# Kernel optimization log

Measured on AMD Instinct MI355X. Metric: run time of the kernel, lower is better.

## Reference

```python
import jax, jax.numpy as jnp
import numpy as np

N, E, D_LM, H, L, C = 100000, 1000000, 1024, 128, 3, 8


def setup_inputs() -> dict:
    key = jax.random.key(0)
    ks = jax.random.split(key, 8)
    return {
        "last_hidden_state": jax.random.normal(ks[0], (N, D_LM), jnp.float32),
        "edge_index": jax.random.randint(ks[1], (2, E), 0, N, dtype=jnp.int32),
        "W_lm": jax.random.normal(ks[2], (D_LM, H), jnp.float32) * 0.03,
        "b_lm": jnp.zeros((H,), jnp.float32),
        "W_gcn": jax.random.normal(ks[3], (L, H, H), jnp.float32) * 0.08,
        "b_gcn": jnp.zeros((L, H), jnp.float32),
        "W_cls": jax.random.normal(ks[4], (2 * H, C), jnp.float32) * 0.06,
        "b_cls": jnp.zeros((C,), jnp.float32),
    }


def reference(last_hidden_state, edge_index, W_lm, b_lm, W_gcn, b_gcn, W_cls, b_cls):
    # Frozen LM output -> lm_head (dropout is identity in eval mode)
    n = last_hidden_state.shape[0]
    lm = last_hidden_state @ W_lm + b_lm                      # [N, H]

    # GCN normalization (add self-loops, symmetric deg^{-1/2} norm), shared by all layers
    loops = jnp.arange(n, dtype=edge_index.dtype)
    src = jnp.concatenate([edge_index[0], loops])             # message sources j
    dst = jnp.concatenate([edge_index[1], loops])             # aggregation targets i
    deg = jax.ops.segment_sum(jnp.ones_like(dst, jnp.float32), dst, num_segments=n)
    dinv = jax.lax.rsqrt(jnp.maximum(deg, 1.0))               # deg >= 1 due to self-loops
    norm = dinv[src] * dinv[dst]                              # [E+N]

    out = lm
    for l in range(W_gcn.shape[0]):
        h = out @ W_gcn[l]                                    # linear transform first (PyG GCNConv)
        msg = h[src] * norm[:, None]                          # gather + scale  [E+N, H]
        out = jax.ops.segment_sum(msg, dst, num_segments=n) + b_gcn[l]
        out = jax.nn.relu(out)                                # dropout identity in eval

    logits = jnp.concatenate([lm, out], axis=-1) @ W_cls + b_cls  # [N, C]
    return logits
```

## Files before the change

### kernel.cpp

```cpp
#include <hip/hip_runtime.h>


using bf16x8 = __attribute__((ext_vector_type(8))) short;
using f32x4  = __attribute__((ext_vector_type(4))) float;
typedef unsigned short u16;
typedef unsigned int   u32;

__device__ __forceinline__ u16 f2bf(float f) {
  u32 u = __builtin_bit_cast(u32, f);
  u += 0x7fffu + ((u >> 16) & 1u);
  return (u16)(u >> 16);
}
__device__ __forceinline__ float bf2f(u32 lo16) {
  return __builtin_bit_cast(float, lo16 << 16);
}
__device__ __forceinline__ u32 packbf2(float a, float b) {
  return (u32)f2bf(a) | ((u32)f2bf(b) << 16);
}


__global__ void count_kernel(const int* __restrict__ dst, int* __restrict__ counts, int E) {
  int e = blockIdx.x * 256 + threadIdx.x;
  if (e < E) atomicAdd(&counts[dst[e]], 1);
}

__global__ void dinv_kernel(const int* __restrict__ counts, float* __restrict__ dinv, int N) {
  int i = blockIdx.x * 256 + threadIdx.x;
  if (i < N) dinv[i] = rsqrtf((float)(counts[i] + 1));
}

__global__ void scan_partial(const int* __restrict__ counts, int* __restrict__ partials, int N) {
  __shared__ int sdata[256];
  int t = threadIdx.x;
  int base = blockIdx.x * 1024 + t * 4;
  int s = 0;
#pragma unroll
  for (int i = 0; i < 4; i++) { int idx = base + i; if (idx < N) s += counts[idx]; }
  sdata[t] = s; __syncthreads();
  for (int off = 128; off > 0; off >>= 1) {
    if (t < off) sdata[t] += sdata[t + off];
    __syncthreads();
  }
  if (t == 0) partials[blockIdx.x] = sdata[0];
}

__global__ void scan_partials_excl(int* __restrict__ partials, int NB,
                                   int* __restrict__ offsets, int N, int E) {
  __shared__ int sdata[256];
  int t = threadIdx.x;
  int v = (t < NB) ? partials[t] : 0;
  sdata[t] = v; __syncthreads();
  int val = v;
  for (int off = 1; off < 256; off <<= 1) {
    int add = (t >= off) ? sdata[t - off] : 0;
    __syncthreads();
    val += add; sdata[t] = val;
    __syncthreads();
  }
  if (t < NB) partials[t] = val - v;
  if (t == 0) offsets[N] = E;
}

__global__ void scan_final(const int* __restrict__ counts, const int* __restrict__ partials,
                           int* __restrict__ offsets, int N) {
  __shared__ int sdata[256];
  int t = threadIdx.x;
  int base = blockIdx.x * 1024 + t * 4;
  int v[4]; int tsum = 0;
#pragma unroll
  for (int i = 0; i < 4; i++) { int idx = base + i; v[i] = (idx < N) ? counts[idx] : 0; tsum += v[i]; }
  sdata[t] = tsum; __syncthreads();
  int val = tsum;
  for (int off = 1; off < 256; off <<= 1) {
    int add = (t >= off) ? sdata[t - off] : 0;
    __syncthreads();
    val += add; sdata[t] = val;
    __syncthreads();
  }
  int run = partials[blockIdx.x] + val - tsum;
#pragma unroll
  for (int i = 0; i < 4; i++) { int idx = base + i; if (idx < N) offsets[idx] = run; run += v[i]; }
}

__global__ void fill_kernel(const int* __restrict__ src, const int* __restrict__ dst,
                            const int* __restrict__ offsets, int* __restrict__ cursor,
                            const float* __restrict__ dinv,
                            int* __restrict__ col, float* __restrict__ wn, int E) {
  int e = blockIdx.x * 256 + threadIdx.x;
  if (e < E) {
    int d = dst[e], s = src[e];
    int p = offsets[d] + atomicAdd(&cursor[d], 1);
    col[p] = s;
    wn[p] = dinv[s] * dinv[d];
  }
}


__global__ void prep_wlm(const float* __restrict__ W, u16* __restrict__ Wt) {
  int idx = blockIdx.x * 256 + threadIdx.x;
  if (idx < 1024 * 128) {
    int k = idx >> 7, c = idx & 127;
    Wt[c * 1024 + k] = f2bf(W[idx]);
  }
}
__global__ void prep_wgcn(const float* __restrict__ W, u16* __restrict__ Wt, int total) {
  int idx = blockIdx.x * 256 + threadIdx.x;
  if (idx < total) {
    int l = idx >> 14; int r = idx & 16383;
    int k = r >> 7, c = r & 127;
    Wt[l * 16384 + c * 128 + k] = f2bf(W[idx]);
  }
}


template<int K, bool A_IS_F32, bool ADD_BIAS>
__global__ __launch_bounds__(256) void gemm_kernel(
    const void* __restrict__ Aptr, const u16* __restrict__ Bt,
    const float* __restrict__ bias, u16* __restrict__ Out, int Nrows)
{
  __shared__ u16 lA[128 * 32];
  __shared__ u16 lB[128 * 32];
  const int t = threadIdx.x;
  const int lane = t & 63;
  const int w = t >> 6;
  const int wr = w >> 1, wc = w & 1;
  const int row0 = blockIdx.x * 128;
  const int quad = lane >> 4;
  const int l16 = lane & 15;

  f32x4 acc[4][4];
#pragma unroll
  for (int i = 0; i < 4; i++)
#pragma unroll
    for (int j = 0; j < 4; j++) acc[i][j] = f32x4{0.f, 0.f, 0.f, 0.f};

  for (int k0 = 0; k0 < K; k0 += 32) {
    if (A_IS_F32) {
      const float* A = (const float*)Aptr;
#pragma unroll
      for (int rpt = 0; rpt < 2; rpt++) {
        int seg = t + rpt * 256;
        int row = seg >> 2, ks = seg & 3;
        int grow = row0 + row; if (grow >= Nrows) grow = Nrows - 1;
        const float* gp = A + (size_t)grow * K + k0 + ks * 8;
        float4 f0 = *reinterpret_cast<const float4*>(gp);
        float4 f1 = *reinterpret_cast<const float4*>(gp + 4);
        uint4 pk;
        pk.x = packbf2(f0.x, f0.y); pk.y = packbf2(f0.z, f0.w);
        pk.z = packbf2(f1.x, f1.y); pk.w = packbf2(f1.z, f1.w);
        *reinterpret_cast<uint4*>(&lA[seg * 8]) = pk;
      }
    } else {
      const u16* A = (const u16*)Aptr;
#pragma unroll
      for (int rpt = 0; rpt < 2; rpt++) {
        int seg = t + rpt * 256;
        int row = seg >> 2, ks = seg & 3;
        int grow = row0 + row; if (grow >= Nrows) grow = Nrows - 1;
        const u16* gp = A + (size_t)grow * K + k0 + ks * 8;
        *reinterpret_cast<uint4*>(&lA[seg * 8]) = *reinterpret_cast<const uint4*>(gp);
      }
    }
#pragma unroll
    for (int rpt = 0; rpt < 2; rpt++) {
      int seg = t + rpt * 256;
      int c = seg >> 2, ks = seg & 3;
      const u16* gp = Bt + (size_t)c * K + k0 + ks * 8;
      *reinterpret_cast<uint4*>(&lB[seg * 8]) = *reinterpret_cast<const uint4*>(gp);
    }
    __syncthreads();

    bf16x8 af[4], bfr[4];
#pragma unroll
    for (int i = 0; i < 4; i++) {
      int r = wr * 64 + i * 16 + l16;
      af[i] = *reinterpret_cast<const bf16x8*>(&lA[r * 32 + quad * 8]);
    }
#pragma unroll
    for (int j = 0; j < 4; j++) {
      int c = wc * 64 + j * 16 + l16;
      bfr[j] = *reinterpret_cast<const bf16x8*>(&lB[c * 32 + quad * 8]);
    }
    __syncthreads();

#pragma unroll
    for (int i = 0; i < 4; i++)
#pragma unroll
      for (int j = 0; j < 4; j++)
        acc[i][j] = __builtin_amdgcn_mfma_f32_16x16x32_bf16(af[i], bfr[j], acc[i][j], 0, 0, 0);
  }

#pragma unroll
  for (int i = 0; i < 4; i++) {
    int rbase = row0 + wr * 64 + i * 16 + quad * 4;
#pragma unroll
    for (int j = 0; j < 4; j++) {
      int c = wc * 64 + j * 16 + l16;
      float bv = ADD_BIAS ? bias[c] : 0.f;
#pragma unroll
      for (int r = 0; r < 4; r++) {
        int grow = rbase + r;
        if (grow < Nrows) {
          float v = acc[i][j][r] + bv;
          Out[(size_t)grow * 128 + c] = f2bf(v);
        }
      }
    }
  }
}


__global__ __launch_bounds__(256) void aggregate_kernel(
    const u16* __restrict__ h, const int* __restrict__ offsets,
    const int* __restrict__ col, const float* __restrict__ wn,
    const float* __restrict__ dinv, const float* __restrict__ bias,
    u16* __restrict__ outf, int N)
{
  int w = threadIdx.x >> 6;
  int lane = threadIdx.x & 63;
  int i = blockIdx.x * 4 + w;
  if (i >= N) return;
  const u32* h32 = (const u32*)h;
  float di = dinv[i];
  float sw = di * di;
  u32 us = h32[(size_t)i * 64 + lane];
  float ax = sw * bf2f(us & 0xffffu);
  float ay = sw * bf2f(us >> 16);
  int s = offsets[i], e = offsets[i + 1];
  int p = s;
  for (; p + 4 <= e; p += 4) {
    int j0 = col[p], j1 = col[p + 1], j2 = col[p + 2], j3 = col[p + 3];
    float w0 = wn[p], w1 = wn[p + 1], w2 = wn[p + 2], w3 = wn[p + 3];
    u32 u0 = h32[(size_t)j0 * 64 + lane];
    u32 u1 = h32[(size_t)j1 * 64 + lane];
    u32 u2 = h32[(size_t)j2 * 64 + lane];
    u32 u3 = h32[(size_t)j3 * 64 + lane];
    ax += w0 * bf2f(u0 & 0xffffu); ay += w0 * bf2f(u0 >> 16);
    ax += w1 * bf2f(u1 & 0xffffu); ay += w1 * bf2f(u1 >> 16);
    ax += w2 * bf2f(u2 & 0xffffu); ay += w2 * bf2f(u2 >> 16);
    ax += w3 * bf2f(u3 & 0xffffu); ay += w3 * bf2f(u3 >> 16);
  }
  for (; p < e; p++) {
    int j = col[p]; float wv = wn[p];
    u32 uu = h32[(size_t)j * 64 + lane];
    ax += wv * bf2f(uu & 0xffffu); ay += wv * bf2f(uu >> 16);
  }
  ax = fmaxf(ax + bias[lane * 2], 0.f);
  ay = fmaxf(ay + bias[lane * 2 + 1], 0.f);
  ((u32*)outf)[(size_t)i * 64 + lane] = packbf2(ax, ay);
}


__global__ __launch_bounds__(256) void classifier_kernel(
    const u16* __restrict__ lm, const u16* __restrict__ feat,
    const float* __restrict__ Wc, const float* __restrict__ bc,
    float* __restrict__ out, int N)
{
  __shared__ float sW[256 * 8];
  __shared__ u16 sF[32 * 264];
  int t = threadIdx.x;
#pragma unroll
  for (int r = 0; r < 8; r++) sW[t + r * 256] = Wc[t + r * 256];
  int n0 = blockIdx.x * 32;
  u32* sF32 = (u32*)sF;
#pragma unroll
  for (int r = 0; r < 8; r++) {
    int idx = t + r * 256;
    int n = idx >> 6, cpos = idx & 63;
    int gn = n0 + n; if (gn >= N) gn = N - 1;
    sF32[n * 132 + cpos]      = ((const u32*)lm)[(size_t)gn * 64 + cpos];
    sF32[n * 132 + 64 + cpos] = ((const u32*)feat)[(size_t)gn * 64 + cpos];
  }
  __syncthreads();
  int n = t >> 3, c = t & 7;
  int gn = n0 + n;
  float sum = bc[c];
#pragma unroll 16
  for (int k = 0; k < 256; k++)
    sum += bf2f((u32)sF[n * 264 + k]) * sW[k * 8 + c];
  if (gn < N) out[(size_t)gn * 8 + c] = sum;
}


static inline char* bump(char*& p, size_t bytes) {
  char* r = p;
  p += (bytes + 255) & ~(size_t)255;
  return r;
}

extern "C" void kernel_launch(void* const* d_in, const int* in_sizes, int n_in,
                              void* d_out, int out_size, void* d_ws, size_t ws_size,
                              hipStream_t stream) {
  const float* X   = (const float*)d_in[0];
  const int*   EI  = (const int*)  d_in[1];
  const float* Wlm = (const float*)d_in[2];
  const float* blm = (const float*)d_in[3];
  const float* Wg  = (const float*)d_in[4];
  const float* bg  = (const float*)d_in[5];
  const float* Wc  = (const float*)d_in[6];
  const float* bc  = (const float*)d_in[7];
  float* out = (float*)d_out;

  const int N = in_sizes[0] / 1024;
  const int E = in_sizes[1] / 2;
  const int L = in_sizes[4] / (128 * 128);

  char* wp = (char*)d_ws;
  int*   counts  = (int*)  bump(wp, (size_t)N * 4);
  int*   cursor  = (int*)  bump(wp, (size_t)N * 4);
  int*   offs    = (int*)  bump(wp, (size_t)(N + 1) * 4);
  float* dinv    = (float*)bump(wp, (size_t)N * 4);
  int*   partials= (int*)  bump(wp, 1024 * 4);
  int*   colA    = (int*)  bump(wp, (size_t)E * 4);
  float* wnA     = (float*)bump(wp, (size_t)E * 4);
  u16*   WlmT    = (u16*)  bump(wp, (size_t)1024 * 128 * 2);
  u16*   WgT     = (u16*)  bump(wp, (size_t)L * 128 * 128 * 2);
  u16*   lmB     = (u16*)  bump(wp, (size_t)N * 128 * 2);
  u16*   hB      = (u16*)  bump(wp, (size_t)N * 128 * 2);
  u16*   featB   = (u16*)  bump(wp, (size_t)N * 128 * 2);

  hipMemsetAsync(counts, 0, (size_t)N * 4, stream);
  hipMemsetAsync(cursor, 0, (size_t)N * 4, stream);

  const int* srcp = EI;
  const int* dstp = EI + E;

  count_kernel<<<(E + 255) / 256, 256, 0, stream>>>(dstp, counts, E);
  dinv_kernel<<<(N + 255) / 256, 256, 0, stream>>>(counts, dinv, N);

  int NB = (N + 1023) / 1024;
  scan_partial<<<NB, 256, 0, stream>>>(counts, partials, N);
  scan_partials_excl<<<1, 256, 0, stream>>>(partials, NB, offs, N, E);
  scan_final<<<NB, 256, 0, stream>>>(counts, partials, offs, N);
  fill_kernel<<<(E + 255) / 256, 256, 0, stream>>>(srcp, dstp, offs, cursor, dinv, colA, wnA, E);

  prep_wlm<<<(1024 * 128 + 255) / 256, 256, 0, stream>>>(Wlm, WlmT);
  prep_wgcn<<<(L * 128 * 128 + 255) / 256, 256, 0, stream>>>(Wg, WgT, L * 128 * 128);

  int GB = (N + 127) / 128;
  gemm_kernel<1024, true, true><<<GB, 256, 0, stream>>>(X, WlmT, blm, lmB, N);

  const u16* cur = lmB;
  for (int l = 0; l < L; l++) {
    gemm_kernel<128, false, false><<<GB, 256, 0, stream>>>(cur, WgT + (size_t)l * 16384, nullptr, hB, N);
    aggregate_kernel<<<(N + 3) / 4, 256, 0, stream>>>(hB, offs, colA, wnA, dinv, bg + (size_t)l * 128, featB, N);
    cur = featB;
  }

  classifier_kernel<<<(N + 31) / 32, 256, 0, stream>>>(lmB, featB, Wc, bc, out, N);
}
```

Measured before the change: 984.4 us.

## Fuse GCN aggregation and transform per layer, switch to fp16 MFMA

Each GCN layer now aggregates first (A·X) into shared memory and then applies the 128x128 weight with MFMA in a single kernel. This reorders the math from (A·(XW)) to ((A·X)W), removing the separate per-layer GEMM launch and the round trip of the intermediate h buffer through global memory. Storage and MFMA move from bf16 to fp16, B fragments are read straight from global/L2 instead of being staged in LDS, and the two weight-prep kernels are merged into one. The risks are fp16 range and precision issues and lower occupancy from the 512-thread blocks with a large LDS tile.

New measurement: 1.169 ms. +18.8%, slower.

```diff
diff --git a/kernel.cpp b/kernel.cpp
--- a/kernel.cpp
+++ b/kernel.cpp
@@ -1,22 +1,21 @@
 #include <hip/hip_runtime.h>
 
 
-using bf16x8 = __attribute__((ext_vector_type(8))) short;
-using f32x4  = __attribute__((ext_vector_type(4))) float;
 typedef unsigned short u16;
 typedef unsigned int   u32;
-
-__device__ __forceinline__ u16 f2bf(float f) {
-  u32 u = __builtin_bit_cast(u32, f);
-  u += 0x7fffu + ((u >> 16) & 1u);
-  return (u16)(u >> 16);
-}
-__device__ __forceinline__ float bf2f(u32 lo16) {
-  return __builtin_bit_cast(float, lo16 << 16);
-}
-__device__ __forceinline__ u32 packbf2(float a, float b) {
-  return (u32)f2bf(a) | ((u32)f2bf(b) << 16);
-}
+typedef _Float16 f16;
+typedef f16 f16x8 __attribute__((ext_vector_type(8)));
+typedef f16 f16x2 __attribute__((ext_vector_type(2)));
+typedef __fp16 fp16x2_storage __attribute__((ext_vector_type(2)));
+typedef float f32x4 __attribute__((ext_vector_type(4)));
+
+__device__ __forceinline__ u32 pkh2(float a, float b) {
+  fp16x2_storage h = __builtin_amdgcn_cvt_pkrtz(a, b);
+  return __builtin_bit_cast(u32, h);
+}
+__device__ __forceinline__ float h2f_lo(u32 u) { return (float)__builtin_bit_cast(f16x2, u)[0]; }
+__device__ __forceinline__ float h2f_hi(u32 u) { return (float)__builtin_bit_cast(f16x2, u)[1]; }
+__device__ __forceinline__ u16 f2h(float f) { return __builtin_bit_cast(u16, (f16)f); }
 
 
 __global__ void count_kernel(const int* __restrict__ dst, int* __restrict__ counts, int E) {
@@ -96,30 +95,27 @@
 }
 
 
-__global__ void prep_wlm(const float* __restrict__ W, u16* __restrict__ Wt) {
+__global__ void prep_weights(const float* __restrict__ Wlm, const float* __restrict__ Wg,
+                             f16* __restrict__ WlmT, f16* __restrict__ WgT, int total) {
   int idx = blockIdx.x * 256 + threadIdx.x;
   if (idx < 1024 * 128) {
     int k = idx >> 7, c = idx & 127;
-    Wt[c * 1024 + k] = f2bf(W[idx]);
-  }
-}
-__global__ void prep_wgcn(const float* __restrict__ W, u16* __restrict__ Wt, int total) {
-  int idx = blockIdx.x * 256 + threadIdx.x;
-  if (idx < total) {
-    int l = idx >> 14; int r = idx & 16383;
-    int k = r >> 7, c = r & 127;
-    Wt[l * 16384 + c * 128 + k] = f2bf(W[idx]);
-  }
-}
-
-
-template<int K, bool A_IS_F32, bool ADD_BIAS>
-__global__ __launch_bounds__(256) void gemm_kernel(
-    const void* __restrict__ Aptr, const u16* __restrict__ Bt,
+    WlmT[c * 1024 + k] = (f16)Wlm[idx];
+  } else if (idx < total) {
+    int r = idx - 1024 * 128;
+    int l = r >> 14; int rr = r & 16383;
+    int k = rr >> 7, c = rr & 127;
+    WgT[l * 16384 + c * 128 + k] = (f16)Wg[r];
+  }
+}
+
+
+template<int K>
+__global__ __launch_bounds__(256) void lm_gemm_kernel(
+    const float* __restrict__ A, const f16* __restrict__ Bt,
     const float* __restrict__ bias, u16* __restrict__ Out, int Nrows)
 {
   __shared__ u16 lA[128 * 32];
-  __shared__ u16 lB[128 * 32];
   const int t = threadIdx.x;
   const int lane = t & 63;
   const int w = t >> 6;
@@ -135,51 +131,31 @@
     for (int j = 0; j < 4; j++) acc[i][j] = f32x4{0.f, 0.f, 0.f, 0.f};
 
   for (int k0 = 0; k0 < K; k0 += 32) {
-    if (A_IS_F32) {
-      const float* A = (const float*)Aptr;
-#pragma unroll
-      for (int rpt = 0; rpt < 2; rpt++) {
-        int seg = t + rpt * 256;
-        int row = seg >> 2, ks = seg & 3;
-        int grow = row0 + row; if (grow >= Nrows) grow = Nrows - 1;
-        const float* gp = A + (size_t)grow * K + k0 + ks * 8;
-        float4 f0 = *reinterpret_cast<const float4*>(gp);
-        float4 f1 = *reinterpret_cast<const float4*>(gp + 4);
-        uint4 pk;
-        pk.x = packbf2(f0.x, f0.y); pk.y = packbf2(f0.z, f0.w);
-        pk.z = packbf2(f1.x, f1.y); pk.w = packbf2(f1.z, f1.w);
-        *reinterpret_cast<uint4*>(&lA[seg * 8]) = pk;
-      }
-    } else {
-      const u16* A = (const u16*)Aptr;
-#pragma unroll
-      for (int rpt = 0; rpt < 2; rpt++) {
-        int seg = t + rpt * 256;
-        int row = seg >> 2, ks = seg & 3;
-        int grow = row0 + row; if (grow >= Nrows) grow = Nrows - 1;
-        const u16* gp = A + (size_t)grow * K + k0 + ks * 8;
-        *reinterpret_cast<uint4*>(&lA[seg * 8]) = *reinterpret_cast<const uint4*>(gp);
-      }
-    }
 #pragma unroll
     for (int rpt = 0; rpt < 2; rpt++) {
       int seg = t + rpt * 256;
-      int c = seg >> 2, ks = seg & 3;
-      const u16* gp = Bt + (size_t)c * K + k0 + ks * 8;
-      *reinterpret_cast<uint4*>(&lB[seg * 8]) = *reinterpret_cast<const uint4*>(gp);
-    }
-    __syncthreads();
-
-    bf16x8 af[4], bfr[4];
+      int row = seg >> 2, ks = seg & 3;
+      int grow = row0 + row; if (grow >= Nrows) grow = Nrows - 1;
+      const float* gp = A + (size_t)grow * K + k0 + ks * 8;
+      float4 f0 = *reinterpret_cast<const float4*>(gp);
+      float4 f1 = *reinterpret_cast<const float4*>(gp + 4);
+      uint4 pk;
+      pk.x = pkh2(f0.x, f0.y); pk.y = pkh2(f0.z, f0.w);
+      pk.z = pkh2(f1.x, f1.y); pk.w = pkh2(f1.z, f1.w);
+      *reinterpret_cast<uint4*>(&lA[seg * 8]) = pk;
+    }
+    __syncthreads();
+
+    f16x8 af[4], bfr[4];
 #pragma unroll
     for (int i = 0; i < 4; i++) {
       int r = wr * 64 + i * 16 + l16;
-      af[i] = *reinterpret_cast<const bf16x8*>(&lA[r * 32 + quad * 8]);
+      af[i] = *reinterpret_cast<const f16x8*>(&lA[r * 32 + quad * 8]);
     }
 #pragma unroll
     for (int j = 0; j < 4; j++) {
       int c = wc * 64 + j * 16 + l16;
-      bfr[j] = *reinterpret_cast<const bf16x8*>(&lB[c * 32 + quad * 8]);
+      bfr[j] = *reinterpret_cast<const f16x8*>(Bt + (size_t)c * K + k0 + quad * 8);
     }
     __syncthreads();
 
@@ -187,7 +163,7 @@
     for (int i = 0; i < 4; i++)
 #pragma unroll
       for (int j = 0; j < 4; j++)
-        acc[i][j] = __builtin_amdgcn_mfma_f32_16x16x32_bf16(af[i], bfr[j], acc[i][j], 0, 0, 0);
+        acc[i][j] = __builtin_amdgcn_mfma_f32_16x16x32_f16(af[i], bfr[j], acc[i][j], 0, 0, 0);
   }
 
 #pragma unroll
@@ -196,58 +172,88 @@
 #pragma unroll
     for (int j = 0; j < 4; j++) {
       int c = wc * 64 + j * 16 + l16;
-      float bv = ADD_BIAS ? bias[c] : 0.f;
+      float bv = bias[c];
 #pragma unroll
       for (int r = 0; r < 4; r++) {
         int grow = rbase + r;
-        if (grow < Nrows) {
-          float v = acc[i][j][r] + bv;
-          Out[(size_t)grow * 128 + c] = f2bf(v);
-        }
+        if (grow < Nrows) Out[(size_t)grow * 128 + c] = f2h(acc[i][j][r] + bv);
       }
     }
   }
 }
 
 
-__global__ __launch_bounds__(256) void aggregate_kernel(
-    const u16* __restrict__ h, const int* __restrict__ offsets,
+__global__ __launch_bounds__(512) void gcn_layer_kernel(
+    const u16* __restrict__ Hin, const int* __restrict__ offs,
     const int* __restrict__ col, const float* __restrict__ wn,
-    const float* __restrict__ dinv, const float* __restrict__ bias,
-    u16* __restrict__ outf, int N)
+    const float* __restrict__ dinv, const f16* __restrict__ Wt,
+    const float* __restrict__ bias, u16* __restrict__ Hout, int N)
 {
-  int w = threadIdx.x >> 6;
-  int lane = threadIdx.x & 63;
-  int i = blockIdx.x * 4 + w;
-  if (i >= N) return;
-  const u32* h32 = (const u32*)h;
-  float di = dinv[i];
-  float sw = di * di;
-  u32 us = h32[(size_t)i * 64 + lane];
-  float ax = sw * bf2f(us & 0xffffu);
-  float ay = sw * bf2f(us >> 16);
-  int s = offsets[i], e = offsets[i + 1];
-  int p = s;
-  for (; p + 4 <= e; p += 4) {
-    int j0 = col[p], j1 = col[p + 1], j2 = col[p + 2], j3 = col[p + 3];
-    float w0 = wn[p], w1 = wn[p + 1], w2 = wn[p + 2], w3 = wn[p + 3];
-    u32 u0 = h32[(size_t)j0 * 64 + lane];
-    u32 u1 = h32[(size_t)j1 * 64 + lane];
-    u32 u2 = h32[(size_t)j2 * 64 + lane];
-    u32 u3 = h32[(size_t)j3 * 64 + lane];
-    ax += w0 * bf2f(u0 & 0xffffu); ay += w0 * bf2f(u0 >> 16);
-    ax += w1 * bf2f(u1 & 0xffffu); ay += w1 * bf2f(u1 >> 16);
-    ax += w2 * bf2f(u2 & 0xffffu); ay += w2 * bf2f(u2 >> 16);
-    ax += w3 * bf2f(u3 & 0xffffu); ay += w3 * bf2f(u3 >> 16);
-  }
-  for (; p < e; p++) {
-    int j = col[p]; float wv = wn[p];
-    u32 uu = h32[(size_t)j * 64 + lane];
-    ax += wv * bf2f(uu & 0xffffu); ay += wv * bf2f(uu >> 16);
-  }
-  ax = fmaxf(ax + bias[lane * 2], 0.f);
-  ay = fmaxf(ay + bias[lane * 2 + 1], 0.f);
-  ((u32*)outf)[(size_t)i * 64 + lane] = packbf2(ax, ay);
+  __shared__ u16 lA[128 * 136];
+  const int t = threadIdx.x;
+  const int lane = t & 63;
+  const int w = t >> 6;
+  const int row0 = blockIdx.x * 128;
+  const u32* h32 = (const u32*)Hin;
+  u32* lA32 = (u32*)lA;
+
+  for (int r = w; r < 128; r += 8) {
+    int i = row0 + r;
+    float ax = 0.f, ay = 0.f;
+    if (i < N) {
+      float di = dinv[i];
+      float sw = di * di;
+      u32 us = h32[(size_t)i * 64 + lane];
+      ax = sw * h2f_lo(us); ay = sw * h2f_hi(us);
+      int e = offs[i + 1];
+      int p = offs[i];
+      for (; p + 4 <= e; p += 4) {
+        int j0 = col[p], j1 = col[p + 1], j2 = col[p + 2], j3 = col[p + 3];
+        float w0 = wn[p], w1 = wn[p + 1], w2 = wn[p + 2], w3 = wn[p + 3];
+        u32 u0 = h32[(size_t)j0 * 64 + lane];
+        u32 u1 = h32[(size_t)j1 * 64 + lane];
+        u32 u2 = h32[(size_t)j2 * 64 + lane];
+        u32 u3 = h32[(size_t)j3 * 64 + lane];
+        ax += w0 * h2f_lo(u0); ay += w0 * h2f_hi(u0);
+        ax += w1 * h2f_lo(u1); ay += w1 * h2f_hi(u1);
+        ax += w2 * h2f_lo(u2); ay += w2 * h2f_hi(u2);
+        ax += w3 * h2f_lo(u3); ay += w3 * h2f_hi(u3);
+      }
+      for (; p < e; p++) {
+        int j = col[p]; float wv = wn[p];
+        u32 uu = h32[(size_t)j * 64 + lane];
+        ax += wv * h2f_lo(uu); ay += wv * h2f_hi(uu);
+      }
+    }
+    lA32[r * 68 + lane] = pkh2(ax, ay);
+  }
+  __syncthreads();
+
+  const int l16 = lane & 15, quad = lane >> 4;
+  f32x4 acc[8];
+#pragma unroll
+  for (int j = 0; j < 8; j++) acc[j] = f32x4{0.f, 0.f, 0.f, 0.f};
+
+#pragma unroll
+  for (int k0 = 0; k0 < 128; k0 += 32) {
+    f16x8 af = *reinterpret_cast<const f16x8*>(&lA[(w * 16 + l16) * 136 + k0 + quad * 8]);
+#pragma unroll
+    for (int j = 0; j < 8; j++) {
+      f16x8 bf = *reinterpret_cast<const f16x8*>(Wt + (size_t)(j * 16 + l16) * 128 + k0 + quad * 8);
+      acc[j] = __builtin_amdgcn_mfma_f32_16x16x32_f16(af, bf, acc[j], 0, 0, 0);
+    }
+  }
+
+#pragma unroll
+  for (int j = 0; j < 8; j++) {
+    int c = j * 16 + l16;
+    float bv = bias[c];
+#pragma unroll
+    for (int r = 0; r < 4; r++) {
+      int grow = row0 + w * 16 + quad * 4 + r;
+      if (grow < N) Hout[(size_t)grow * 128 + c] = f2h(fmaxf(acc[j][r] + bv, 0.f));
+    }
+  }
 }
 
 
@@ -274,10 +280,11 @@
   __syncthreads();
   int n = t >> 3, c = t & 7;
   int gn = n0 + n;
+  const f16* sFh = (const f16*)sF;
   float sum = bc[c];
 #pragma unroll 16
   for (int k = 0; k < 256; k++)
-    sum += bf2f((u32)sF[n * 264 + k]) * sW[k * 8 + c];
+    sum += (float)sFh[n * 264 + k] * sW[k * 8 + c];
   if (gn < N) out[(size_t)gn * 8 + c] = sum;
 }
 
@@ -313,14 +320,14 @@
   int*   partials= (int*)  bump(wp, 1024 * 4);
   int*   colA    = (int*)  bump(wp, (size_t)E * 4);
   float* wnA     = (float*)bump(wp, (size_t)E * 4);
-  u16*   WlmT    = (u16*)  bump(wp, (size_t)1024 * 128 * 2);
-  u16*   WgT     = (u16*)  bump(wp, (size_t)L * 128 * 128 * 2);
+  f16*   WlmT    = (f16*)  bump(wp, (size_t)1024 * 128 * 2);
+  f16*   WgT     = (f16*)  bump(wp, (size_t)L * 128 * 128 * 2);
   u16*   lmB     = (u16*)  bump(wp, (size_t)N * 128 * 2);
-  u16*   hB      = (u16*)  bump(wp, (size_t)N * 128 * 2);
-  u16*   featB   = (u16*)  bump(wp, (size_t)N * 128 * 2);
-
-  hipMemsetAsync(counts, 0, (size_t)N * 4, stream);
-  hipMemsetAsync(cursor, 0, (size_t)N * 4, stream);
+  u16*   fA      = (u16*)  bump(wp, (size_t)N * 128 * 2);
+  u16*   fB      = (u16*)  bump(wp, (size_t)N * 128 * 2);
+
+  (void)hipMemsetAsync(counts, 0, (size_t)N * 4, stream);
+  (void)hipMemsetAsync(cursor, 0, (size_t)N * 4, stream);
 
   const int* srcp = EI;
   const int* dstp = EI + E;
@@ -334,18 +341,20 @@
   scan_final<<<NB, 256, 0, stream>>>(counts, partials, offs, N);
   fill_kernel<<<(E + 255) / 256, 256, 0, stream>>>(srcp, dstp, offs, cursor, dinv, colA, wnA, E);
 
-  prep_wlm<<<(1024 * 128 + 255) / 256, 256, 0, stream>>>(Wlm, WlmT);
-  prep_wgcn<<<(L * 128 * 128 + 255) / 256, 256, 0, stream>>>(Wg, WgT, L * 128 * 128);
+  int PT = 1024 * 128 + L * 128 * 128;
+  prep_weights<<<(PT + 255) / 256, 256, 0, stream>>>(Wlm, Wg, WlmT, WgT, PT);
 
   int GB = (N + 127) / 128;
-  gemm_kernel<1024, true, true><<<GB, 256, 0, stream>>>(X, WlmT, blm, lmB, N);
+  lm_gemm_kernel<1024><<<GB, 256, 0, stream>>>(X, WlmT, blm, lmB, N);
 
   const u16* cur = lmB;
+  u16* bufs[3] = {fA, fB, fA};
   for (int l = 0; l < L; l++) {
-    gemm_kernel<128, false, false><<<GB, 256, 0, stream>>>(cur, WgT + (size_t)l * 16384, nullptr, hB, N);
-    aggregate_kernel<<<(N + 3) / 4, 256, 0, stream>>>(hB, offs, colA, wnA, dinv, bg + (size_t)l * 128, featB, N);
-    cur = featB;
-  }
-
-  classifier_kernel<<<(N + 31) / 32, 256, 0, stream>>>(lmB, featB, Wc, bc, out, N);
-}
+    u16* dst = bufs[l % 3];
+    gcn_layer_kernel<<<GB, 512, 0, stream>>>(cur, offs, colA, wnA, dinv,
+                                             WgT + (size_t)l * 16384, bg + (size_t)l * 128, dst, N);
+    cur = dst;
+  }
+
+  classifier_kernel<<<(N + 31) / 32, 256, 0, stream>>>(lmB, cur, Wc, bc, out, N);
+}
```
